# Kernel tuning notes

Measured on AMD Instinct MI355X. Metric: run time of the kernel, lower is better.

## Reference

```python
import jax, jax.numpy as jnp
import numpy as np

N_NODES = 50000
N_EDGES = 800000
IN_FEATS = 96
H_FEATS = 256
N_HOPS = 3
N_NIE = N_HOPS + 1  # hops 0..3
NDIM_FC = N_NIE * H_FEATS


def setup_inputs() -> dict:
    key = jax.random.key(0)
    ks = jax.random.split(key, 8)
    edge_index = jax.random.randint(ks[0], (2, N_EDGES), 0, N_NODES, dtype=jnp.int64)
    features = jax.random.normal(ks[1], (N_NODES, IN_FEATS), dtype=jnp.float32)
    # per-hop MLP params: Linear(in_feats, h_feats) for each of n_nie hops
    s_in = 1.0 / np.sqrt(IN_FEATS)
    Ws = jax.random.uniform(ks[2], (N_NIE, IN_FEATS, H_FEATS), jnp.float32, -s_in, s_in)
    bs = jax.random.uniform(ks[3], (N_NIE, H_FEATS), jnp.float32, -s_in, s_in)
    # fusion: Linear(ndim_fc, h_feats)
    s_fc = 1.0 / np.sqrt(NDIM_FC)
    Wf = jax.random.uniform(ks[4], (NDIM_FC, H_FEATS), jnp.float32, -s_fc, s_fc)
    bf = jax.random.uniform(ks[5], (H_FEATS,), jnp.float32, -s_fc, s_fc)
    return {"edge_index": edge_index, "features": features, "Ws": Ws, "bs": bs, "Wf": Wf, "bf": bf}


def _build_norm_adj(edge_index):
    """set_diag (remove existing diag, add unit self-loops) + symmetric D^-1/2 A D^-1/2.
    Returns (rows, cols, edge_w) COO of the normalized adjacency."""
    row, col = edge_index[0].astype(jnp.int32), edge_index[1].astype(jnp.int32)
    loop = jnp.arange(N_NODES, dtype=jnp.int32)
    rows = jnp.concatenate([row, loop])
    cols = jnp.concatenate([col, loop])
    # zero out any pre-existing diagonal entries, self-loops get weight 1 (set_diag semantics)
    w = jnp.concatenate([(row != col).astype(jnp.float32), jnp.ones((N_NODES,), jnp.float32)])
    deg = jax.ops.segment_sum(w, rows, num_segments=N_NODES)
    dinv = jnp.where(deg > 0, jax.lax.rsqrt(deg), 0.0)
    edge_w = dinv[rows] * w * dinv[cols]
    return rows, cols, edge_w


def _spmm(rows, cols, edge_w, x):
    # out[r] = sum_e w_e * x[cols[e]] for edges with rows[e]==r
    return jax.ops.segment_sum(edge_w[:, None] * x[cols], rows, num_segments=N_NODES)


def reference(edge_index, features, Ws, bs, Wf, bf):
    rows, cols, edge_w = _build_norm_adj(edge_index)
    # row-normalize features (F.normalize dim=1)
    x = features / jnp.maximum(jnp.linalg.norm(features, axis=1, keepdims=True), 1e-12)
    nei_feats = [x]
    h = x
    for _ in range(N_HOPS):
        h = _spmm(rows, cols, edge_w, h)
        nei_feats.append(h)
    # per-hop MLP (dropout p=0 -> identity; norm=None -> identity) then ReLU
    ns = [jax.nn.relu(nei_feats[i] @ Ws[i] + bs[i]) for i in range(N_NIE)]
    cat = jnp.concatenate(ns, axis=1)  # [N, ndim_fc]
    out = jax.nn.relu(cat @ Wf + bf)   # [N, h_feats]
    return out
```

## Files before the change

### kernel.cpp

```cpp
#include <hip/hip_runtime.h>

#define N_NODES 50000
#define N_EDGES 800000
#define IN_F 96
#define H_F 256
#define N_NIE 4
#define SCAN_NB 196
#define BM 64
#define NBLK 782
#define LDA1 104

typedef float f32x4 __attribute__((ext_vector_type(4)));
typedef short s16x8 __attribute__((ext_vector_type(8)));
typedef unsigned short ushort;

__device__ __forceinline__ ushort bf16_rne(float f) {
    unsigned u = __float_as_uint(f);
    u += 0x7fffu + ((u >> 16) & 1u);
    return (ushort)(u >> 16);
}
__device__ __forceinline__ float bf16_f(ushort h) {
    return __uint_as_float(((unsigned)h) << 16);
}

__global__ __launch_bounds__(256) void k_count(const int* __restrict__ rows,
                                               const int* __restrict__ cols,
                                               int* __restrict__ cnt) {
    int i = blockIdx.x * 256 + threadIdx.x;
    if (i >= N_EDGES / 2) return;
    int2 r2 = ((const int2*)rows)[i];
    int2 c2 = ((const int2*)cols)[i];
    if (r2.x != c2.x) atomicAdd(&cnt[r2.x], 1);
    if (r2.y != c2.y) atomicAdd(&cnt[r2.y], 1);
}

__global__ __launch_bounds__(256) void k_scan1(const int* __restrict__ cnt,
                                               int* __restrict__ rowptr,
                                               int* __restrict__ bsum) {
    __shared__ int s[256];
    int t = threadIdx.x, e = blockIdx.x * 256 + t;
    int v = (e < N_NODES) ? cnt[e] : 0;
    s[t] = v;
    __syncthreads();
    #pragma unroll
    for (int off = 1; off < 256; off <<= 1) {
        int nv = (t >= off) ? s[t - off] : 0;
        __syncthreads();
        s[t] += nv;
        __syncthreads();
    }
    if (e < N_NODES) rowptr[e] = s[t] - v;
    if (t == 255) bsum[blockIdx.x] = s[255];
}

__global__ __launch_bounds__(256) void k_scan2(int* __restrict__ bsum,
                                               int* __restrict__ boff,
                                               int* __restrict__ rowptr) {
    __shared__ int s[256];
    int t = threadIdx.x;
    int v = (t < SCAN_NB) ? bsum[t] : 0;
    s[t] = v;
    __syncthreads();
    #pragma unroll
    for (int off = 1; off < 256; off <<= 1) {
        int nv = (t >= off) ? s[t - off] : 0;
        __syncthreads();
        s[t] += nv;
        __syncthreads();
    }
    if (t < SCAN_NB) boff[t] = s[t] - v;
    if (t == 255) rowptr[N_NODES] = s[255];
}

__global__ __launch_bounds__(256) void k_scan3(const int* __restrict__ boff,
                                               const int* __restrict__ cnt,
                                               int* __restrict__ rowptr,
                                               int* __restrict__ cursor,
                                               float* __restrict__ dinv) {
    int e = blockIdx.x * 256 + threadIdx.x;
    if (e >= N_NODES) return;
    int r = rowptr[e] + boff[blockIdx.x];
    rowptr[e] = r;
    cursor[e] = r;
    dinv[e] = rsqrtf((float)cnt[e] + 1.0f);
}

__global__ __launch_bounds__(256) void k_scatter(const int* __restrict__ rows,
                                                 const int* __restrict__ cols,
                                                 int* __restrict__ cursor,
                                                 int* __restrict__ cwi) {
    int e = blockIdx.x * 256 + threadIdx.x;
    if (e >= N_EDGES) return;
    int r = rows[e], c = cols[e];
    if (r == c) return;
    int p = atomicAdd(&cursor[r], 1);
    __builtin_nontemporal_store(c, &cwi[p]);
}

__global__ __launch_bounds__(256) void k_wsplit_ws(const float* __restrict__ src,
                                                   ushort* __restrict__ dst) {
    int idx = blockIdx.x * 256 + threadIdx.x;
    if (idx >= N_NIE * IN_F * H_F) return;
    int hop = idx / (IN_F * H_F), rem = idx % (IN_F * H_F);
    int k = rem / H_F, n = rem % H_F;
    int c = n >> 6, wc = (n >> 5) & 1, b = (n >> 4) & 1, rsel = n & 15;
    int ks = k >> 5, kk = k & 31;
    int lane = (kk >> 3) * 16 + rsel, sel8 = kk & 7;
    int d = (((((hop * 4 + c) * 2 + wc) * 2 + b) * 3 + ks) * 64 + lane) * 8 + sel8;
    dst[d] = bf16_rne(src[idx]);
}

__global__ __launch_bounds__(256) void k_wsplit_wf(const float* __restrict__ src,
                                                   ushort* __restrict__ dst) {
    int idx = blockIdx.x * 256 + threadIdx.x;
    if (idx >= N_NIE * H_F * H_F) return;
    int hop = idx / (H_F * H_F), rem = idx % (H_F * H_F);
    int k = rem / H_F, n = rem % H_F;
    int kc = k >> 5, kk = k & 31;
    int w = n >> 5, rem2 = n & 31;
    int cf = rem2 >> 4, rsel = rem2 & 15;
    int lane = (kk >> 3) * 16 + rsel, sel8 = kk & 7;
    int d = ((((hop * 8 + kc) * 8 + w) * 2 + cf) * 64 + lane) * 8 + sel8;
    dst[d] = bf16_rne(src[idx]);
}

__global__ __launch_bounds__(256) void k_norm(const float* __restrict__ feat,
                                              ushort* __restrict__ x) {
    int wid = (blockIdx.x * 256 + threadIdx.x) >> 6;
    int lane = threadIdx.x & 63;
    if (wid >= N_NODES) return;
    const float* fr = feat + (size_t)wid * IN_F;
    float v0 = (lane < IN_F) ? fr[lane] : 0.0f;
    float v1 = (lane < IN_F - 64) ? fr[64 + lane] : 0.0f;
    float ss = v0 * v0 + v1 * v1;
    #pragma unroll
    for (int o = 32; o; o >>= 1) ss += __shfl_xor(ss, o, 64);
    float inv = 1.0f / fmaxf(sqrtf(ss), 1e-12f);
    ushort* xr = x + (size_t)wid * IN_F;
    if (lane < IN_F) xr[lane] = bf16_rne(v0 * inv);
    if (lane < IN_F - 64) xr[64 + lane] = bf16_rne(v1 * inv);
}

__global__ __launch_bounds__(256) void k_spmm_csr(const int* __restrict__ rowptr,
                                                  const int* __restrict__ cwi,
                                                  const float* __restrict__ dinv,
                                                  const ushort* __restrict__ x,
                                                  ushort* __restrict__ y) {
    int g = (blockIdx.x * 256 + threadIdx.x) >> 4;
    if (g >= N_NODES) return;
    int l = threadIdx.x & 15;
    bool act = l < 12;
    float dr = dinv[g];
    s16x8 sv = {0, 0, 0, 0, 0, 0, 0, 0};
    if (act) sv = *(const s16x8*)&x[(size_t)g * IN_F + l * 8];
    float a[8] = {}, b[8] = {};
    int k = rowptr[g], e = rowptr[g + 1];
    for (; k + 3 < e; k += 4) {
        int c0 = cwi[k], c1 = cwi[k + 1], c2 = cwi[k + 2], c3 = cwi[k + 3];
        float w0 = dinv[c0], w1 = dinv[c1], w2 = dinv[c2], w3 = dinv[c3];
        s16x8 v0 = {0, 0, 0, 0, 0, 0, 0, 0}, v1 = v0, v2 = v0, v3 = v0;
        if (act) {
            v0 = *(const s16x8*)&x[(size_t)c0 * IN_F + l * 8];
            v1 = *(const s16x8*)&x[(size_t)c1 * IN_F + l * 8];
            v2 = *(const s16x8*)&x[(size_t)c2 * IN_F + l * 8];
            v3 = *(const s16x8*)&x[(size_t)c3 * IN_F + l * 8];
        }
        #pragma unroll
        for (int q = 0; q < 8; ++q) {
            a[q] += bf16_f((ushort)v0[q]) * w0 + bf16_f((ushort)v1[q]) * w1;
            b[q] += bf16_f((ushort)v2[q]) * w2 + bf16_f((ushort)v3[q]) * w3;
        }
    }
    for (; k < e; ++k) {
        int c0 = cwi[k];
        float w0 = dinv[c0];
        s16x8 v0 = {0, 0, 0, 0, 0, 0, 0, 0};
        if (act) v0 = *(const s16x8*)&x[(size_t)c0 * IN_F + l * 8];
        #pragma unroll
        for (int q = 0; q < 8; ++q) a[q] += bf16_f((ushort)v0[q]) * w0;
    }
    if (act) {
        s16x8 o;
        #pragma unroll
        for (int q = 0; q < 8; ++q)
            o[q] = (short)bf16_rne(dr * ((a[q] + b[q]) + dr * bf16_f((ushort)sv[q])));
        *(s16x8*)&y[(size_t)g * IN_F + l * 8] = o;
    }
}

__global__ __launch_bounds__(512, 4) void k_mega(const ushort* __restrict__ h0,
                                                 const ushort* __restrict__ h1,
                                                 const ushort* __restrict__ h2,
                                                 const ushort* __restrict__ h3,
                                                 const ushort* __restrict__ Ws2,
                                                 const float* __restrict__ bs,
                                                 const ushort* __restrict__ Wf2,
                                                 const float* __restrict__ bf,
                                                 float* __restrict__ out) {
    __shared__ ushort SM[23040];
    ushort* nsH = SM;
    ushort* Ah  = SM + 16384;
    float* T = (float*)SM;

    int m0 = blockIdx.x * BM;
    int tid = threadIdx.x;
    int lane = tid & 63, w = tid >> 6;
    int rsel = lane & 15, g = lane >> 4, ksel = g * 8;
    int crow = g * 4, ccol = rsel;
    int rw0 = (w & 3) * 16;
    int wc = w >> 2;
    int cwb = wc * 32;

    int sr0 = tid / 12, sj0 = tid - sr0 * 12;
    int f1 = tid + 512;
    int sr1 = f1 / 12, sj1 = f1 - sr1 * 12;

    f32x4 acc[4][2] = {};

    for (int hop = 0; hop < N_NIE; ++hop) {
        const ushort* A = (hop == 0) ? h0 : (hop == 1) ? h1 : (hop == 2) ? h2 : h3;
        const ushort* wsF = Ws2 + (size_t)hop * IN_F * H_F;
        const ushort* wfF = Wf2 + (size_t)hop * H_F * H_F;
        const float* bsi = bs + hop * H_F;

        {
            int gm = m0 + sr0;
            s16x8 v = {0, 0, 0, 0, 0, 0, 0, 0};
            if (gm < N_NODES) v = *(const s16x8*)&A[(size_t)gm * IN_F + sj0 * 8];
            *(s16x8*)&Ah[sr0 * LDA1 + sj0 * 8] = v;
            if (tid < 256) {
                int gm1 = m0 + sr1;
                s16x8 v1 = {0, 0, 0, 0, 0, 0, 0, 0};
                if (gm1 < N_NODES) v1 = *(const s16x8*)&A[(size_t)gm1 * IN_F + sj1 * 8];
                *(s16x8*)&Ah[sr1 * LDA1 + sj1 * 8] = v1;
            }
        }
        __syncthreads();
        #pragma unroll
        for (int c = 0; c < 4; ++c) {
            const ushort* bsrc = wsF + (size_t)((c * 2 + wc) * 2) * 3 * 64 * 8;
            f32x4 ac[2] = {};
            __builtin_amdgcn_s_setprio(1);
            #pragma unroll
            for (int ks = 0; ks < 3; ++ks) {
                s16x8 ah = *(const s16x8*)&Ah[(rw0 + rsel) * LDA1 + ks * 32 + ksel];
                s16x8 b0 = *(const s16x8*)&bsrc[(size_t)(ks * 64 + lane) * 8];
                s16x8 b1 = *(const s16x8*)&bsrc[(size_t)((3 + ks) * 64 + lane) * 8];
                ac[0] = __builtin_amdgcn_mfma_f32_16x16x32_bf16(ah, b0, ac[0], 0, 0, 0);
                ac[1] = __builtin_amdgcn_mfma_f32_16x16x32_bf16(ah, b1, ac[1], 0, 0, 0);
            }
            __builtin_amdgcn_s_setprio(0);
            #pragma unroll
            for (int cf = 0; cf < 2; ++cf) {
                int col = c * 64 + cwb + cf * 16 + ccol;
                float bb = bsi[col];
                #pragma unroll
                for (int ii = 0; ii < 4; ++ii) {
                    int row = rw0 + crow + ii;
                    nsH[row * 256 + (col ^ ((row & 7) << 3))] =
                        bf16_rne(fmaxf(ac[cf][ii] + bb, 0.f));
                }
            }
        }
        __syncthreads();
        #pragma unroll
        for (int kc = 0; kc < 8; ++kc) {
            int k0 = kc * 32 + ksel;
            s16x8 ah4[4];
            #pragma unroll
            for (int rf = 0; rf < 4; ++rf) {
                int row = rf * 16 + rsel;
                ah4[rf] = *(const s16x8*)&nsH[row * 256 + (k0 ^ ((row & 7) << 3))];
            }
            __builtin_amdgcn_s_setprio(1);
            #pragma unroll
            for (int cf = 0; cf < 2; ++cf) {
                s16x8 bh = *(const s16x8*)&wfF[(size_t)(((kc * 8 + w) * 2 + cf) * 64 + lane) * 8];
                #pragma unroll
                for (int rf = 0; rf < 4; ++rf)
                    acc[rf][cf] = __builtin_amdgcn_mfma_f32_16x16x32_bf16(ah4[rf], bh, acc[rf][cf], 0, 0, 0);
            }
            __builtin_amdgcn_s_setprio(0);
        }
        __syncthreads();
    }
    #pragma unroll
    for (int half = 0; half < 2; ++half) {
        __syncthreads();
        #pragma unroll
        for (int rf2 = 0; rf2 < 2; ++rf2) {
            int rf = half * 2 + rf2;
            #pragma unroll
            for (int cf = 0; cf < 2; ++cf) {
                int col = w * 32 + cf * 16 + ccol;
                #pragma unroll
                for (int ii = 0; ii < 4; ++ii)
                    T[(rf2 * 16 + crow + ii) * 260 + col] = acc[rf][cf][ii];
            }
        }
        __syncthreads();
        #pragma unroll
        for (int p = 0; p < 4; ++p) {
            int flat = tid + p * 512;
            int r = flat >> 6, jc = flat & 63;
            int gm = m0 + half * 32 + r;
            if (gm < N_NODES) {
                f32x4 v = *(f32x4*)&T[r * 260 + jc * 4];
                f32x4 bb = *(const f32x4*)&bf[jc * 4];
                f32x4 o;
                #pragma unroll
                for (int q = 0; q < 4; ++q) o[q] = fmaxf(v[q] + bb[q], 0.f);
                *(f32x4*)&out[(size_t)gm * H_F + jc * 4] = o;
            }
        }
    }
}

extern "C" void kernel_launch(void* const* d_in, const int* in_sizes, int n_in,
                              void* d_out, int out_size, void* d_ws, size_t ws_size,
                              hipStream_t stream) {
    const int* ei = (const int*)d_in[0];
    const int* rows = ei;
    const int* cols = ei + N_EDGES;
    const float* feat = (const float*)d_in[1];
    const float* Ws = (const float*)d_in[2];
    const float* bs = (const float*)d_in[3];
    const float* Wf = (const float*)d_in[4];
    const float* bf = (const float*)d_in[5];
    float* out = (float*)d_out;

    ushort* h0 = (ushort*)d_ws;
    ushort* h1 = h0 + (size_t)N_NODES * IN_F;
    ushort* h2 = h1 + (size_t)N_NODES * IN_F;
    ushort* h3 = h2 + (size_t)N_NODES * IN_F;
    ushort* Ws2 = h3 + (size_t)N_NODES * IN_F;
    ushort* Wf2 = Ws2 + N_NIE * IN_F * H_F;
    float* dinv = (float*)(Wf2 + N_NIE * H_F * H_F);
    int* rowptr = (int*)(dinv + N_NODES);
    int* bsum = rowptr + 50004;
    int* boff = bsum + 256;
    int* cwi = boff + 256;
    int* cnt = (int*)h1;
    int* cursor = cnt + N_NODES;

    hipMemsetAsync(cnt, 0, N_NODES * sizeof(int), stream);
    k_count<<<(N_EDGES / 2 + 255) / 256, 256, 0, stream>>>(rows, cols, cnt);
    k_scan1<<<SCAN_NB, 256, 0, stream>>>(cnt, rowptr, bsum);
    k_scan2<<<1, 256, 0, stream>>>(bsum, boff, rowptr);
    k_scan3<<<SCAN_NB, 256, 0, stream>>>(boff, cnt, rowptr, cursor, dinv);
    k_scatter<<<(N_EDGES + 255) / 256, 256, 0, stream>>>(rows, cols, cursor, cwi);
    k_wsplit_ws<<<(N_NIE * IN_F * H_F + 255) / 256, 256, 0, stream>>>(Ws, Ws2);
    k_wsplit_wf<<<(N_NIE * H_F * H_F + 255) / 256, 256, 0, stream>>>(Wf, Wf2);
    k_norm<<<(N_NODES + 3) / 4, 256, 0, stream>>>(feat, h0);

    k_spmm_csr<<<(N_NODES * 16 + 255) / 256, 256, 0, stream>>>(rowptr, cwi, dinv, h0, h1);
    k_spmm_csr<<<(N_NODES * 16 + 255) / 256, 256, 0, stream>>>(rowptr, cwi, dinv, h1, h2);
    k_spmm_csr<<<(N_NODES * 16 + 255) / 256, 256, 0, stream>>>(rowptr, cwi, dinv, h2, h3);
    k_mega<<<NBLK, 512, 0, stream>>>(h0, h1, h2, h3, Ws2, bs, Wf2, bf, out);
}
```

Before: 308.6 us.

## Make each wave own 16 rows in fused MLP kernel, removing block barriers

The fused per-hop MLP kernel now runs 256 threads per block, and each wave owns a 16-row strip across all 256 output columns. It loads its A fragments directly from global memory into registers and keeps its intermediate activations in a private LDS slice. All __syncthreads barriers and the shared A staging are gone, and the weight-permutation kernels are rewritten to match the new fragment order. In exchange, each wave now reads the full Ws/Wf weight sets with no sharing across waves, which raises L2 traffic per row. The accumulator array grows to 16 fragments, which adds register pressure.

```diff
diff --git a/kernel.cpp b/kernel.cpp
--- a/kernel.cpp
+++ b/kernel.cpp
@@ -6,9 +6,7 @@
 #define H_F 256
 #define N_NIE 4
 #define SCAN_NB 196
-#define BM 64
 #define NBLK 782
-#define LDA1 104
 
 typedef float f32x4 __attribute__((ext_vector_type(4)));
 typedef short s16x8 __attribute__((ext_vector_type(8)));
@@ -103,10 +101,10 @@
     if (idx >= N_NIE * IN_F * H_F) return;
     int hop = idx / (IN_F * H_F), rem = idx % (IN_F * H_F);
     int k = rem / H_F, n = rem % H_F;
-    int c = n >> 6, wc = (n >> 5) & 1, b = (n >> 4) & 1, rsel = n & 15;
+    int cf = n >> 4;
     int ks = k >> 5, kk = k & 31;
-    int lane = (kk >> 3) * 16 + rsel, sel8 = kk & 7;
-    int d = (((((hop * 4 + c) * 2 + wc) * 2 + b) * 3 + ks) * 64 + lane) * 8 + sel8;
+    int lane = (kk >> 3) * 16 + (n & 15), sel8 = kk & 7;
+    int d = (((hop * 16 + cf) * 3 + ks) * 64 + lane) * 8 + sel8;
     dst[d] = bf16_rne(src[idx]);
 }
 
@@ -117,10 +115,9 @@
     int hop = idx / (H_F * H_F), rem = idx % (H_F * H_F);
     int k = rem / H_F, n = rem % H_F;
     int kc = k >> 5, kk = k & 31;
-    int w = n >> 5, rem2 = n & 31;
-    int cf = rem2 >> 4, rsel = rem2 & 15;
-    int lane = (kk >> 3) * 16 + rsel, sel8 = kk & 7;
-    int d = ((((hop * 8 + kc) * 8 + w) * 2 + cf) * 64 + lane) * 8 + sel8;
+    int cf = n >> 4;
+    int lane = (kk >> 3) * 16 + (n & 15), sel8 = kk & 7;
+    int d = (((hop * 8 + kc) * 16 + cf) * 64 + lane) * 8 + sel8;
     dst[d] = bf16_rne(src[idx]);
 }
 
@@ -188,7 +185,7 @@
     }
 }
 
-__global__ __launch_bounds__(512, 4) void k_mega(const ushort* __restrict__ h0,
+__global__ __launch_bounds__(256, 4) void k_mega(const ushort* __restrict__ h0,
                                                  const ushort* __restrict__ h1,
                                                  const ushort* __restrict__ h2,
                                                  const ushort* __restrict__ h3,
@@ -197,25 +194,16 @@
                                                  const ushort* __restrict__ Wf2,
                                                  const float* __restrict__ bf,
                                                  float* __restrict__ out) {
-    __shared__ ushort SM[23040];
-    ushort* nsH = SM;
-    ushort* Ah  = SM + 16384;
-    float* T = (float*)SM;
-
-    int m0 = blockIdx.x * BM;
+    __shared__ ushort SM[16384];
     int tid = threadIdx.x;
-    int lane = tid & 63, w = tid >> 6;
+    int lane = tid & 63, wv = tid >> 6;
+    ushort* myNs = SM + wv * 4096;
     int rsel = lane & 15, g = lane >> 4, ksel = g * 8;
     int crow = g * 4, ccol = rsel;
-    int rw0 = (w & 3) * 16;
-    int wc = w >> 2;
-    int cwb = wc * 32;
-
-    int sr0 = tid / 12, sj0 = tid - sr0 * 12;
-    int f1 = tid + 512;
-    int sr1 = f1 / 12, sj1 = f1 - sr1 * 12;
-
-    f32x4 acc[4][2] = {};
+    int row0 = blockIdx.x * 64 + wv * 16;
+    int arow = row0 + rsel;
+
+    f32x4 acc[16] = {};
 
     for (int hop = 0; hop < N_NIE; ++hop) {
         const ushort* A = (hop == 0) ? h0 : (hop == 1) ? h1 : (hop == 2) ? h2 : h3;
@@ -223,94 +211,61 @@
         const ushort* wfF = Wf2 + (size_t)hop * H_F * H_F;
         const float* bsi = bs + hop * H_F;
 
-        {
-            int gm = m0 + sr0;
+        s16x8 af[3];
+        #pragma unroll
+        for (int ks = 0; ks < 3; ++ks) {
             s16x8 v = {0, 0, 0, 0, 0, 0, 0, 0};
-            if (gm < N_NODES) v = *(const s16x8*)&A[(size_t)gm * IN_F + sj0 * 8];
-            *(s16x8*)&Ah[sr0 * LDA1 + sj0 * 8] = v;
-            if (tid < 256) {
-                int gm1 = m0 + sr1;
-                s16x8 v1 = {0, 0, 0, 0, 0, 0, 0, 0};
-                if (gm1 < N_NODES) v1 = *(const s16x8*)&A[(size_t)gm1 * IN_F + sj1 * 8];
-                *(s16x8*)&Ah[sr1 * LDA1 + sj1 * 8] = v1;
-            }
-        }
-        __syncthreads();
-        #pragma unroll
-        for (int c = 0; c < 4; ++c) {
-            const ushort* bsrc = wsF + (size_t)((c * 2 + wc) * 2) * 3 * 64 * 8;
-            f32x4 ac[2] = {};
-            __builtin_amdgcn_s_setprio(1);
+            if (arow < N_NODES) v = *(const s16x8*)&A[(size_t)arow * IN_F + ks * 32 + ksel];
+            af[ks] = v;
+        }
+        #pragma unroll
+        for (int cf = 0; cf < 16; ++cf) {
+            f32x4 ac = {};
             #pragma unroll
             for (int ks = 0; ks < 3; ++ks) {
-                s16x8 ah = *(const s16x8*)&Ah[(rw0 + rsel) * LDA1 + ks * 32 + ksel];
-                s16x8 b0 = *(const s16x8*)&bsrc[(size_t)(ks * 64 + lane) * 8];
-                s16x8 b1 = *(const s16x8*)&bsrc[(size_t)((3 + ks) * 64 + lane) * 8];
-                ac[0] = __builtin_amdgcn_mfma_f32_16x16x32_bf16(ah, b0, ac[0], 0, 0, 0);
-                ac[1] = __builtin_amdgcn_mfma_f32_16x16x32_bf16(ah, b1, ac[1], 0, 0, 0);
+                s16x8 b = *(const s16x8*)&wsF[(size_t)((cf * 3 + ks) * 64 + lane) * 8];
+                ac = __builtin_amdgcn_mfma_f32_16x16x32_bf16(af[ks], b, ac, 0, 0, 0);
             }
-            __builtin_amdgcn_s_setprio(0);
+            int col = cf * 16 + ccol;
+            float bb = bsi[col];
             #pragma unroll
-            for (int cf = 0; cf < 2; ++cf) {
-                int col = c * 64 + cwb + cf * 16 + ccol;
-                float bb = bsi[col];
-                #pragma unroll
-                for (int ii = 0; ii < 4; ++ii) {
-                    int row = rw0 + crow + ii;
-                    nsH[row * 256 + (col ^ ((row & 7) << 3))] =
-                        bf16_rne(fmaxf(ac[cf][ii] + bb, 0.f));
-                }
+            for (int ii = 0; ii < 4; ++ii) {
+                int r = crow + ii;
+                myNs[r * 256 + (col ^ ((r & 7) << 3))] = bf16_rne(fmaxf(ac[ii] + bb, 0.f));
             }
         }
-        __syncthreads();
         #pragma unroll
         for (int kc = 0; kc < 8; ++kc) {
-            int k0 = kc * 32 + ksel;
-            s16x8 ah4[4];
+            s16x8 ah = *(const s16x8*)&myNs[rsel * 256 + ((kc * 32 + ksel) ^ ((rsel & 7) << 3))];
             #pragma unroll
-            for (int rf = 0; rf < 4; ++rf) {
-                int row = rf * 16 + rsel;
-                ah4[rf] = *(const s16x8*)&nsH[row * 256 + (k0 ^ ((row & 7) << 3))];
+            for (int cf = 0; cf < 16; ++cf) {
+                s16x8 b = *(const s16x8*)&wfF[(size_t)((kc * 16 + cf) * 64 + lane) * 8];
+                acc[cf] = __builtin_amdgcn_mfma_f32_16x16x32_bf16(ah, b, acc[cf], 0, 0, 0);
             }
-            __builtin_amdgcn_s_setprio(1);
-            #pragma unroll
-            for (int cf = 0; cf < 2; ++cf) {
-                s16x8 bh = *(const s16x8*)&wfF[(size_t)(((kc * 8 + w) * 2 + cf) * 64 + lane) * 8];
-                #pragma unroll
-                for (int rf = 0; rf < 4; ++rf)
-                    acc[rf][cf] = __builtin_amdgcn_mfma_f32_16x16x32_bf16(ah4[rf], bh, acc[rf][cf], 0, 0, 0);
-            }
-            __builtin_amdgcn_s_setprio(0);
-        }
-        __syncthreads();
-    }
+        }
+    }
+    float* T = (float*)myNs;
     #pragma unroll
     for (int half = 0; half < 2; ++half) {
-        __syncthreads();
-        #pragma unroll
-        for (int rf2 = 0; rf2 < 2; ++rf2) {
-            int rf = half * 2 + rf2;
+        #pragma unroll
+        for (int cf = 0; cf < 8; ++cf) {
+            int col = cf * 16 + ccol;
             #pragma unroll
-            for (int cf = 0; cf < 2; ++cf) {
-                int col = w * 32 + cf * 16 + ccol;
-                #pragma unroll
-                for (int ii = 0; ii < 4; ++ii)
-                    T[(rf2 * 16 + crow + ii) * 260 + col] = acc[rf][cf][ii];
-            }
-        }
-        __syncthreads();
-        #pragma unroll
-        for (int p = 0; p < 4; ++p) {
-            int flat = tid + p * 512;
-            int r = flat >> 6, jc = flat & 63;
-            int gm = m0 + half * 32 + r;
+            for (int ii = 0; ii < 4; ++ii)
+                T[(crow + ii) * 128 + col] = acc[half * 8 + cf][ii];
+        }
+        #pragma unroll
+        for (int q = 0; q < 8; ++q) {
+            int idx = lane + q * 64;
+            int r = idx >> 5, jc = idx & 31;
+            int gm = row0 + r;
             if (gm < N_NODES) {
-                f32x4 v = *(f32x4*)&T[r * 260 + jc * 4];
-                f32x4 bb = *(const f32x4*)&bf[jc * 4];
+                f32x4 v = *(f32x4*)&T[r * 128 + jc * 4];
+                f32x4 bb = *(const f32x4*)&bf[half * 128 + jc * 4];
                 f32x4 o;
                 #pragma unroll
-                for (int q = 0; q < 4; ++q) o[q] = fmaxf(v[q] + bb[q], 0.f);
-                *(f32x4*)&out[(size_t)gm * H_F + jc * 4] = o;
+                for (int q2 = 0; q2 < 4; ++q2) o[q2] = fmaxf(v[q2] + bb[q2], 0.f);
+                *(f32x4*)&out[(size_t)gm * H_F + half * 128 + jc * 4] = o;
             }
         }
     }
@@ -356,5 +311,5 @@
     k_spmm_csr<<<(N_NODES * 16 + 255) / 256, 256, 0, stream>>>(rowptr, cwi, dinv, h0, h1);
     k_spmm_csr<<<(N_NODES * 16 + 255) / 256, 256, 0, stream>>>(rowptr, cwi, dinv, h1, h2);
     k_spmm_csr<<<(N_NODES * 16 + 255) / 256, 256, 0, stream>>>(rowptr, cwi, dinv, h2, h3);
-    k_mega<<<NBLK, 512, 0, stream>>>(h0, h1, h2, h3, Ws2, bs, Wf2, bf, out);
-}
+    k_mega<<<NBLK, 256, 0, stream>>>(h0, h1, h2, h3, Ws2, bs, Wf2, bf, out);
+}
```

New measurement: 411.6 us. +33.4%, slower.
